# Kernel optimization log

Hardware: AMD Instinct MI355X
Metric: run time of the kernel (lower is better)

The kernel has to match this reference:

```python
import jax, jax.numpy as jnp
import numpy as np

WS = 7        # window size
NH = 6        # num heads

def window_partition(x, ws):
    # x: (B, H, W, C) -> (B*nW, ws*ws, C)
    B, H, W, C = x.shape
    x = x.reshape(B, H // ws, ws, W // ws, ws, C)
    x = x.transpose(0, 1, 3, 2, 4, 5)
    return x.reshape(-1, ws * ws, C)

def setup_inputs() -> dict:
    key = jax.random.key(0)
    k1, k2, k3 = jax.random.split(key, 3)
    B, C, H, W = 8, 192, 224, 224
    x = jax.random.normal(k1, (B, C, H, W), dtype=jnp.float32)
    W_qk = jax.random.normal(k2, (2 * C, C), dtype=jnp.float32) * 0.02
    b_qk = jax.random.normal(k3, (2 * C,), dtype=jnp.float32) * 0.02
    return {"x": x, "W_qk": W_qk, "b_qk": b_qk}

def reference(x, W_qk, b_qk):
    B, C, H, W = x.shape
    hd = C // NH
    scale = hd ** (-0.5)
    xw = window_partition(x.transpose(0, 2, 3, 1), WS)      # (BnW, 49, C)
    qk = xw @ W_qk.T + b_qk                                  # (BnW, 49, 2C)
    qk = qk.reshape(-1, WS * WS, 2, NH, hd)
    q = qk[:, :, 0] * scale                                  # (BnW, 49, NH, hd)
    k = qk[:, :, 1]
    attn = jnp.einsum('bnhd,bmhd->bhnm', q, k)               # (BnW, NH, 49, 49)
    return jax.nn.softmax(attn, axis=-1)
```

## Files before the change

kernel.cpp:

```cpp
#include <hip/hip_runtime.h>
#include <hip/hip_bf16.h>
#include <math.h>
#include <stdint.h>

#define CCH   192
#define HWD   224
#define NWIN  8192
#define NPIX  49
#define KDIM  192
#define NHEAD 6
#define ROWB  (KDIM * 2)

typedef __bf16 bf16x8 __attribute__((ext_vector_type(8)));
typedef __bf16 bf16x2 __attribute__((ext_vector_type(2)));
typedef float  f32x4  __attribute__((ext_vector_type(4)));

__global__ void wconv_kernel(const float* __restrict__ w,
                             uint16_t* __restrict__ wbf) {
    int o = blockIdx.x * 256 + threadIdx.x;
    if (o >= 384 * 192) return;
    int e  = o & 7;
    int t  = o >> 3;
    int lr = t & 15;  t >>= 4;
    int lg = t & 3;   t >>= 2;
    int kk = t % 6;
    int ng = t / 6;
    int col  = ng * 16 + lr;
    int kcol = kk * 32 + lg * 8 + e;
    __bf16 v = (__bf16)w[col * KDIM + kcol];
    wbf[o] = __builtin_bit_cast(uint16_t, v);
}

__global__ __launch_bounds__(512, 4)
void attn_win_kernel(const float* __restrict__ x,
                     const uint16_t* __restrict__ wbf,
                     const float* __restrict__ bq,
                     float* __restrict__ out) {
    __shared__ uint16_t ldsA[NPIX * KDIM];
    __shared__ uint16_t ldsB[NPIX * KDIM];

    const int tid  = threadIdx.x;
    const int wave = tid >> 6;
    const int l    = tid & 63;
    const int lg   = l >> 4;
    const int lr   = l & 15;

    const int win = ((blockIdx.x & 7) << 10) | (blockIdx.x >> 3);
    const int b   = win >> 10;
    const int wh  = (win >> 5) & 31;
    const int ww  = win & 31;
    const int h0 = wh * 7, w0 = ww * 7;

    if (l < NPIX) {
        int r = (l * 37) >> 8;
        int s = l - r * 7;
        const float* xp = x + (size_t)(b * CCH + wave * 24) * (HWD * HWD)
                            + (h0 + r) * HWD + (w0 + s);
        const uint32_t rb  = (uint32_t)(l * ROWB + wave * 24 * 2);
        const uint32_t swz = (uint32_t)((l & 7) << 4);
        #pragma unroll 4
        for (int c = 0; c < 24; c += 2) {
            float v0 = xp[0];
            float v1 = xp[HWD * HWD];
            xp += 2 * (HWD * HWD);
            bf16x2 p = { (__bf16)v0, (__bf16)v1 };
            uint32_t byte = (rb + (uint32_t)(c * 2)) ^ swz;
            *(uint32_t*)((char*)ldsA + byte) = __builtin_bit_cast(uint32_t, p);
        }
    }
    __syncthreads();

    f32x4 acc[4][3];
    #pragma unroll
    for (int mt = 0; mt < 4; ++mt)
        #pragma unroll
        for (int nt = 0; nt < 3; ++nt)
            acc[mt][nt] = f32x4{0.f, 0.f, 0.f, 0.f};

    #pragma unroll
    for (int kk = 0; kk < 6; ++kk) {
        bf16x8 afr[4];
        #pragma unroll
        for (int mt = 0; mt < 4; ++mt) {
            int row = mt * 16 + lr;
            if (row > 48) row = 48;
            int byte = (row * ROWB + kk * 64 + lg * 16) ^ ((row & 7) << 4);
            afr[mt] = *(const bf16x8*)((const char*)ldsA + byte);
        }
        #pragma unroll
        for (int nt = 0; nt < 3; ++nt) {
            int ng = wave * 3 + nt;
            bf16x8 bfr = *(const bf16x8*)(wbf + ((ng * 6 + kk) * 4 + lg) * 128 + lr * 8);
            #pragma unroll
            for (int mt = 0; mt < 4; ++mt)
                acc[mt][nt] = __builtin_amdgcn_mfma_f32_16x16x32_bf16(
                    afr[mt], bfr, acc[mt][nt], 0, 0, 0);
        }
    }
    __syncthreads();

    {
        const float mulq = 0.2550348616845977f;
        const bool isq = (wave < 4);
        const float mul = isq ? mulq : 1.0f;
        uint16_t* dst = isq ? ldsA : ldsB;
        #pragma unroll
        for (int nt = 0; nt < 3; ++nt) {
            int colW = wave * 48 + nt * 16 + lr;
            float bias = bq[colW];
            int jj = isq ? colW : (colW - 192);
            #pragma unroll
            for (int mt = 0; mt < 4; ++mt) {
                #pragma unroll
                for (int r = 0; r < 4; ++r) {
                    int row = mt * 16 + lg * 4 + r;
                    if (row < NPIX) {
                        __bf16 bv = (__bf16)((acc[mt][nt][r] + bias) * mul);
                        *(__bf16*)((char*)dst +
                            ((row * ROWB + jj * 2) ^ ((row & 7) << 4))) = bv;
                    }
                }
            }
        }
    }
    __syncthreads();

    float* outw = out + (size_t)win * (NHEAD * NPIX * NPIX);
    const int qt    = wave & 3;
    const int hbase = wave >> 2;
    const int qrow  = qt * 16 + lr;
    const int qrc   = qrow > 48 ? 48 : qrow;
    const uint32_t qswz = (uint32_t)((qrc & 7) << 4);

    for (int hi = 0; hi < 3; ++hi) {
        const int h = hbase + hi * 2;
        const bf16x8 qfr = *(const bf16x8*)((const char*)ldsA +
            (((uint32_t)(qrc * ROWB + h * 64 + lg * 16)) ^ qswz));

        float v[16];
        #pragma unroll
        for (int nt2 = 0; nt2 < 4; ++nt2) {
            int krow = nt2 * 16 + lr;
            if (krow > 48) krow = 48;
            const bf16x8 kfr = *(const bf16x8*)((const char*)ldsB +
                (((uint32_t)(krow * ROWB + h * 64 + lg * 16)) ^ ((krow & 7) << 4)));
            f32x4 p = __builtin_amdgcn_mfma_f32_16x16x32_bf16(
                kfr, qfr, f32x4{0.f, 0.f, 0.f, 0.f}, 0, 0, 0);
            #pragma unroll
            for (int r = 0; r < 4; ++r) {
                int k = nt2 * 16 + lg * 4 + r;
                v[nt2 * 4 + r] = (k < NPIX) ? p[r] : -INFINITY;
            }
        }

        float m = v[0];
        #pragma unroll
        for (int i = 1; i < 16; ++i) m = fmaxf(m, v[i]);
        m = fmaxf(m, __shfl_xor(m, 16, 64));
        m = fmaxf(m, __shfl_xor(m, 32, 64));

        float sum = 0.f;
        #pragma unroll
        for (int i = 0; i < 16; ++i) {
            v[i] = exp2f(v[i] - m);
            sum += v[i];
        }
        sum += __shfl_xor(sum, 16, 64);
        sum += __shfl_xor(sum, 32, 64);
        const float inv = __fdividef(1.0f, sum);

        if (qrow < NPIX) {
            float* orow = outw + h * (NPIX * NPIX) + qrow * NPIX;
            #pragma unroll
            for (int nt2 = 0; nt2 < 3; ++nt2)
                #pragma unroll
                for (int r = 0; r < 4; ++r)
                    orow[nt2 * 16 + lg * 4 + r] = v[nt2 * 4 + r] * inv;
            if (lg == 0) orow[48] = v[12] * inv;
        }
    }
}

extern "C" void kernel_launch(void* const* d_in, const int* in_sizes, int n_in,
                              void* d_out, int out_size, void* d_ws, size_t ws_size,
                              hipStream_t stream) {
    const float* x  = (const float*)d_in[0];
    const float* W  = (const float*)d_in[1];
    const float* bq = (const float*)d_in[2];
    float* out = (float*)d_out;
    uint16_t* wbf = (uint16_t*)d_ws;

    wconv_kernel<<<(384 * 192 + 255) / 256, 256, 0, stream>>>(W, wbf);
    attn_win_kernel<<<NWIN, 512, 0, stream>>>(x, wbf, bq, out);
}
```

Baseline: 336.9 us.

## Process eight windows per block with double-buffered register prefetch of next input

Each block now loops over eight consecutive windows along a row instead of handling one. The next window's input is prefetched from global into registers in two halves, overlapped with the projection GEMM and the softmax phase, and written into a second LDS buffer. A third LDS buffer holds K so Q can overwrite the current input buffer. This hides global load latency and amortizes launch and setup cost, but LDS use grows from two to three buffers, which may lower occupancy, and the grid shrinks eightfold to 1024 blocks.

Measured after the change: 1.269 ms. 3.77x slower.

```diff
diff --git a/kernel.cpp b/kernel.cpp
--- a/kernel.cpp
+++ b/kernel.cpp
@@ -10,6 +10,8 @@
 #define KDIM  192
 #define NHEAD 6
 #define ROWB  (KDIM * 2)
+#define NW    8
+#define NBLK  (NWIN / NW)
 
 typedef __bf16 bf16x8 __attribute__((ext_vector_type(8)));
 typedef __bf16 bf16x2 __attribute__((ext_vector_type(2)));
@@ -36,8 +38,9 @@
                      const uint16_t* __restrict__ wbf,
                      const float* __restrict__ bq,
                      float* __restrict__ out) {
-    __shared__ uint16_t ldsA[NPIX * KDIM];
-    __shared__ uint16_t ldsB[NPIX * KDIM];
+    __shared__ uint16_t bufX[NPIX * KDIM];
+    __shared__ uint16_t bufY[NPIX * KDIM];
+    __shared__ uint16_t bufK[NPIX * KDIM];
 
     const int tid  = threadIdx.x;
     const int wave = tid >> 6;
@@ -45,139 +48,186 @@
     const int lg   = l >> 4;
     const int lr   = l & 15;
 
-    const int win = ((blockIdx.x & 7) << 10) | (blockIdx.x >> 3);
-    const int b   = win >> 10;
-    const int wh  = (win >> 5) & 31;
-    const int ww  = win & 31;
-    const int h0 = wh * 7, w0 = ww * 7;
-
-    if (l < NPIX) {
-        int r = (l * 37) >> 8;
-        int s = l - r * 7;
-        const float* xp = x + (size_t)(b * CCH + wave * 24) * (HWD * HWD)
-                            + (h0 + r) * HWD + (w0 + s);
-        const uint32_t rb  = (uint32_t)(l * ROWB + wave * 24 * 2);
-        const uint32_t swz = (uint32_t)((l & 7) << 4);
-        #pragma unroll 4
+    const int blk  = (int)blockIdx.x;
+    const int blk2 = (blk & 7) * (NBLK / 8) + (blk >> 3);
+    const int wbase = blk2 * NW;
+    const int b    = wbase >> 10;
+    const int wh   = (wbase >> 5) & 31;
+    const int ww0  = wbase & 31;
+    const int h0   = wh * 7;
+
+    const int pr = (l * 37) >> 8;
+    const int ps = l - pr * 7;
+    const float* xlane = x + (size_t)(b * CCH + wave * 24) * (HWD * HWD)
+                           + (size_t)(h0 + pr) * HWD + ps;
+    const uint32_t rb  = (uint32_t)(l * ROWB + wave * 48);
+    const uint32_t swz = (uint32_t)((l & 7) << 4);
+    const bool glane = (l < NPIX);
+
+    if (glane) {
+        const float* xp = xlane + (size_t)(ww0 * 7);
+        #pragma unroll
         for (int c = 0; c < 24; c += 2) {
-            float v0 = xp[0];
-            float v1 = xp[HWD * HWD];
-            xp += 2 * (HWD * HWD);
+            float v0 = xp[(size_t)c * (HWD * HWD)];
+            float v1 = xp[(size_t)(c + 1) * (HWD * HWD)];
             bf16x2 p = { (__bf16)v0, (__bf16)v1 };
-            uint32_t byte = (rb + (uint32_t)(c * 2)) ^ swz;
-            *(uint32_t*)((char*)ldsA + byte) = __builtin_bit_cast(uint32_t, p);
+            *(uint32_t*)((char*)bufX + ((rb + (uint32_t)(c * 2)) ^ swz)) =
+                __builtin_bit_cast(uint32_t, p);
         }
     }
     __syncthreads();
 
-    f32x4 acc[4][3];
-    #pragma unroll
-    for (int mt = 0; mt < 4; ++mt)
+    uint16_t* xc = bufX;
+    uint16_t* xn = bufY;
+
+    for (int j = 0; j < NW; ++j) {
+        const bool pf = (j + 1 < NW) && glane;
+        const float* xpn = xlane + (size_t)((ww0 + j + 1) * 7);
+
+        float ga[12];
+        if (pf) {
+            #pragma unroll
+            for (int c = 0; c < 12; ++c)
+                ga[c] = xpn[(size_t)c * (HWD * HWD)];
+        }
+
+        f32x4 acc[4][3];
         #pragma unroll
-        for (int nt = 0; nt < 3; ++nt)
-            acc[mt][nt] = f32x4{0.f, 0.f, 0.f, 0.f};
-
-    #pragma unroll
-    for (int kk = 0; kk < 6; ++kk) {
-        bf16x8 afr[4];
+        for (int mt = 0; mt < 4; ++mt)
+            #pragma unroll
+            for (int nt = 0; nt < 3; ++nt)
+                acc[mt][nt] = f32x4{0.f, 0.f, 0.f, 0.f};
+
         #pragma unroll
-        for (int mt = 0; mt < 4; ++mt) {
-            int row = mt * 16 + lr;
-            if (row > 48) row = 48;
-            int byte = (row * ROWB + kk * 64 + lg * 16) ^ ((row & 7) << 4);
-            afr[mt] = *(const bf16x8*)((const char*)ldsA + byte);
-        }
-        #pragma unroll
-        for (int nt = 0; nt < 3; ++nt) {
-            int ng = wave * 3 + nt;
-            bf16x8 bfr = *(const bf16x8*)(wbf + ((ng * 6 + kk) * 4 + lg) * 128 + lr * 8);
-            #pragma unroll
-            for (int mt = 0; mt < 4; ++mt)
-                acc[mt][nt] = __builtin_amdgcn_mfma_f32_16x16x32_bf16(
-                    afr[mt], bfr, acc[mt][nt], 0, 0, 0);
-        }
-    }
-    __syncthreads();
-
-    {
-        const float mulq = 0.2550348616845977f;
-        const bool isq = (wave < 4);
-        const float mul = isq ? mulq : 1.0f;
-        uint16_t* dst = isq ? ldsA : ldsB;
-        #pragma unroll
-        for (int nt = 0; nt < 3; ++nt) {
-            int colW = wave * 48 + nt * 16 + lr;
-            float bias = bq[colW];
-            int jj = isq ? colW : (colW - 192);
+        for (int kk = 0; kk < 6; ++kk) {
+            bf16x8 afr[4];
             #pragma unroll
             for (int mt = 0; mt < 4; ++mt) {
-                #pragma unroll
-                for (int r = 0; r < 4; ++r) {
-                    int row = mt * 16 + lg * 4 + r;
-                    if (row < NPIX) {
-                        __bf16 bv = (__bf16)((acc[mt][nt][r] + bias) * mul);
-                        *(__bf16*)((char*)dst +
-                            ((row * ROWB + jj * 2) ^ ((row & 7) << 4))) = bv;
+                int row = mt * 16 + lr;
+                if (row > 48) row = 48;
+                int byte = (row * ROWB + kk * 64 + lg * 16) ^ ((row & 7) << 4);
+                afr[mt] = *(const bf16x8*)((const char*)xc + byte);
+            }
+            #pragma unroll
+            for (int nt = 0; nt < 3; ++nt) {
+                int ng = wave * 3 + nt;
+                bf16x8 bfr = *(const bf16x8*)(wbf + ((ng * 6 + kk) * 4 + lg) * 128 + lr * 8);
+                #pragma unroll
+                for (int mt = 0; mt < 4; ++mt)
+                    acc[mt][nt] = __builtin_amdgcn_mfma_f32_16x16x32_bf16(
+                        afr[mt], bfr, acc[mt][nt], 0, 0, 0);
+            }
+        }
+        __syncthreads();
+
+        if (pf) {
+            #pragma unroll
+            for (int c = 0; c < 12; c += 2) {
+                bf16x2 p = { (__bf16)ga[c], (__bf16)ga[c + 1] };
+                *(uint32_t*)((char*)xn + ((rb + (uint32_t)(c * 2)) ^ swz)) =
+                    __builtin_bit_cast(uint32_t, p);
+            }
+        }
+
+        {
+            const float mulq = 0.2550348616845977f;
+            const bool isq = (wave < 4);
+            const float mul = isq ? mulq : 1.0f;
+            uint16_t* dst = isq ? xc : bufK;
+            #pragma unroll
+            for (int nt = 0; nt < 3; ++nt) {
+                int colW = wave * 48 + nt * 16 + lr;
+                float bias = bq[colW];
+                int jj = isq ? colW : (colW - 192);
+                #pragma unroll
+                for (int mt = 0; mt < 4; ++mt) {
+                    #pragma unroll
+                    for (int r = 0; r < 4; ++r) {
+                        int row = mt * 16 + lg * 4 + r;
+                        if (row < NPIX) {
+                            __bf16 bv = (__bf16)((acc[mt][nt][r] + bias) * mul);
+                            *(__bf16*)((char*)dst +
+                                ((row * ROWB + jj * 2) ^ ((row & 7) << 4))) = bv;
+                        }
                     }
                 }
             }
         }
-    }
-    __syncthreads();
-
-    float* outw = out + (size_t)win * (NHEAD * NPIX * NPIX);
-    const int qt    = wave & 3;
-    const int hbase = wave >> 2;
-    const int qrow  = qt * 16 + lr;
-    const int qrc   = qrow > 48 ? 48 : qrow;
-    const uint32_t qswz = (uint32_t)((qrc & 7) << 4);
-
-    for (int hi = 0; hi < 3; ++hi) {
-        const int h = hbase + hi * 2;
-        const bf16x8 qfr = *(const bf16x8*)((const char*)ldsA +
-            (((uint32_t)(qrc * ROWB + h * 64 + lg * 16)) ^ qswz));
-
-        float v[16];
-        #pragma unroll
-        for (int nt2 = 0; nt2 < 4; ++nt2) {
-            int krow = nt2 * 16 + lr;
-            if (krow > 48) krow = 48;
-            const bf16x8 kfr = *(const bf16x8*)((const char*)ldsB +
-                (((uint32_t)(krow * ROWB + h * 64 + lg * 16)) ^ ((krow & 7) << 4)));
-            f32x4 p = __builtin_amdgcn_mfma_f32_16x16x32_bf16(
-                kfr, qfr, f32x4{0.f, 0.f, 0.f, 0.f}, 0, 0, 0);
-            #pragma unroll
-            for (int r = 0; r < 4; ++r) {
-                int k = nt2 * 16 + lg * 4 + r;
-                v[nt2 * 4 + r] = (k < NPIX) ? p[r] : -INFINITY;
-            }
-        }
-
-        float m = v[0];
-        #pragma unroll
-        for (int i = 1; i < 16; ++i) m = fmaxf(m, v[i]);
-        m = fmaxf(m, __shfl_xor(m, 16, 64));
-        m = fmaxf(m, __shfl_xor(m, 32, 64));
-
-        float sum = 0.f;
-        #pragma unroll
-        for (int i = 0; i < 16; ++i) {
-            v[i] = exp2f(v[i] - m);
-            sum += v[i];
-        }
-        sum += __shfl_xor(sum, 16, 64);
-        sum += __shfl_xor(sum, 32, 64);
-        const float inv = __fdividef(1.0f, sum);
-
-        if (qrow < NPIX) {
-            float* orow = outw + h * (NPIX * NPIX) + qrow * NPIX;
-            #pragma unroll
-            for (int nt2 = 0; nt2 < 3; ++nt2)
-                #pragma unroll
-                for (int r = 0; r < 4; ++r)
-                    orow[nt2 * 16 + lg * 4 + r] = v[nt2 * 4 + r] * inv;
-            if (lg == 0) orow[48] = v[12] * inv;
-        }
+        __syncthreads();
+
+        float gb[12];
+        if (pf) {
+            #pragma unroll
+            for (int c = 0; c < 12; ++c)
+                gb[c] = xpn[(size_t)(12 + c) * (HWD * HWD)];
+        }
+
+        float* outw = out + (size_t)(wbase + j) * (NHEAD * NPIX * NPIX);
+        const int qt    = wave & 3;
+        const int hbase = wave >> 2;
+        const int qrow  = qt * 16 + lr;
+        const int qrc   = qrow > 48 ? 48 : qrow;
+        const uint32_t qswz = (uint32_t)((qrc & 7) << 4);
+
+        for (int hi = 0; hi < 3; ++hi) {
+            const int h = hbase + hi * 2;
+            const bf16x8 qfr = *(const bf16x8*)((const char*)xc +
+                (((uint32_t)(qrc * ROWB + h * 64 + lg * 16)) ^ qswz));
+
+            float v[16];
+            #pragma unroll
+            for (int nt2 = 0; nt2 < 4; ++nt2) {
+                int krow = nt2 * 16 + lr;
+                if (krow > 48) krow = 48;
+                const bf16x8 kfr = *(const bf16x8*)((const char*)bufK +
+                    (((uint32_t)(krow * ROWB + h * 64 + lg * 16)) ^ ((krow & 7) << 4)));
+                f32x4 p = __builtin_amdgcn_mfma_f32_16x16x32_bf16(
+                    kfr, qfr, f32x4{0.f, 0.f, 0.f, 0.f}, 0, 0, 0);
+                #pragma unroll
+                for (int r = 0; r < 4; ++r) {
+                    int k = nt2 * 16 + lg * 4 + r;
+                    v[nt2 * 4 + r] = (k < NPIX) ? p[r] : -INFINITY;
+                }
+            }
+
+            float m = v[0];
+            #pragma unroll
+            for (int i = 1; i < 16; ++i) m = fmaxf(m, v[i]);
+            m = fmaxf(m, __shfl_xor(m, 16, 64));
+            m = fmaxf(m, __shfl_xor(m, 32, 64));
+
+            float sum = 0.f;
+            #pragma unroll
+            for (int i = 0; i < 16; ++i) {
+                v[i] = exp2f(v[i] - m);
+                sum += v[i];
+            }
+            sum += __shfl_xor(sum, 16, 64);
+            sum += __shfl_xor(sum, 32, 64);
+            const float inv = __fdividef(1.0f, sum);
+
+            if (qrow < NPIX) {
+                float* orow = outw + h * (NPIX * NPIX) + qrow * NPIX;
+                #pragma unroll
+                for (int nt2 = 0; nt2 < 3; ++nt2)
+                    #pragma unroll
+                    for (int r = 0; r < 4; ++r)
+                        orow[nt2 * 16 + lg * 4 + r] = v[nt2 * 4 + r] * inv;
+                if (lg == 0) orow[48] = v[12] * inv;
+            }
+        }
+
+        if (pf) {
+            #pragma unroll
+            for (int c = 0; c < 12; c += 2) {
+                bf16x2 p = { (__bf16)gb[c], (__bf16)gb[c + 1] };
+                *(uint32_t*)((char*)xn + ((rb + (uint32_t)((12 + c) * 2)) ^ swz)) =
+                    __builtin_bit_cast(uint32_t, p);
+            }
+        }
+        __syncthreads();
+
+        uint16_t* t = xc; xc = xn; xn = t;
     }
 }
 
@@ -191,5 +241,5 @@
     uint16_t* wbf = (uint16_t*)d_ws;
 
     wconv_kernel<<<(384 * 192 + 255) / 256, 256, 0, stream>>>(W, wbf);
-    attn_win_kernel<<<NWIN, 512, 0, stream>>>(x, wbf, bq, out);
+    attn_win_kernel<<<NBLK, 512, 0, stream>>>(x, wbf, bq, out);
 }
```
